# Kernel optimization log

Measured on AMD Instinct MI355X. Metric: run time of the kernel, lower is better.

The kernel has to match this reference:

```python
import jax, jax.numpy as jnp
import numpy as np

EPS = 1e-3
D_MODEL = 512
SEQ = 1024
BATCH = 4
N_LAYERS = 2
N_HEAD = 8
D_HEAD = 64
D_INNER = 1024


def _position_table(n_pos, d):
    # Faithful to PositionEncoding: sin applied to even cols; the cos line in
    # the source is a no-op (missing assignment), so odd cols stay raw.
    j = np.arange(d)
    pos = np.arange(n_pos)[:, None]
    pe = pos / np.power(10000.0, 2 * (j // 2) / d)
    pe[0] = 0.0
    pe[1:, 0::2] = np.sin(pe[1:, 0::2])
    return jnp.asarray(pe, dtype=jnp.float32)


def _layer_norm(z, a, b):
    # torch.std is unbiased (ddof=1); eps added to sigma, not variance
    mu = jnp.mean(z, axis=-1, keepdims=True)
    sigma = jnp.sqrt(jnp.sum((z - mu) ** 2, axis=-1, keepdims=True) / (z.shape[-1] - 1))
    return (z - mu) / (sigma + EPS) * a + b


def setup_inputs() -> dict:
    key = jax.random.key(0)
    ks = jax.random.split(key, 10)
    s = 0.02
    return {
        "x": jax.random.normal(ks[0], (BATCH, SEQ, D_MODEL), dtype=jnp.float32),
        "pos_enc": _position_table(SEQ, D_MODEL),
        "w_qs": jax.random.normal(ks[1], (N_LAYERS, N_HEAD, D_MODEL, D_HEAD), dtype=jnp.float32) * s,
        "w_ks": jax.random.normal(ks[2], (N_LAYERS, N_HEAD, D_MODEL, D_HEAD), dtype=jnp.float32) * s,
        "w_vs": jax.random.normal(ks[3], (N_LAYERS, N_HEAD, D_MODEL, D_HEAD), dtype=jnp.float32) * s,
        "ln1_a": jnp.ones((N_LAYERS, D_MODEL), dtype=jnp.float32),
        "ln1_b": jnp.zeros((N_LAYERS, D_MODEL), dtype=jnp.float32),
        "w1": jax.random.normal(ks[4], (N_LAYERS, D_INNER, D_MODEL), dtype=jnp.float32) * s,
        "b1": jax.random.normal(ks[5], (N_LAYERS, D_INNER), dtype=jnp.float32) * s,
        "w2": jax.random.normal(ks[6], (N_LAYERS, D_MODEL, D_INNER), dtype=jnp.float32) * s,
        "b2": jax.random.normal(ks[7], (N_LAYERS, D_MODEL), dtype=jnp.float32) * s,
        "ln2_a": jnp.ones((N_LAYERS, D_MODEL), dtype=jnp.float32),
        "ln2_b": jnp.zeros((N_LAYERS, D_MODEL), dtype=jnp.float32),
    }


def reference(x, pos_enc, w_qs, w_ks, w_vs, ln1_a, ln1_b, w1, b1, w2, b2, ln2_a, ln2_b):
    temper = jnp.sqrt(jnp.float32(D_MODEL))  # scale uses d_model, not d_k (as in source)
    x = x + pos_enc[None, :, :]
    for i in range(N_LAYERS):
        residual = x
        # per-head projections: [h, b, l, dk]
        q = jnp.einsum('bld,hdk->hblk', x, w_qs[i])
        k = jnp.einsum('bld,hdk->hblk', x, w_ks[i])
        v = jnp.einsum('bld,hdv->hblv', x, w_vs[i])
        attn = jax.nn.softmax(jnp.einsum('hbqk,hbmk->hbqm', q, k) / temper, axis=-1)
        out = jnp.einsum('hbqm,hbmv->hbqv', attn, v)
        # permute(1,2,0,3): concat heads along feature dim -> [b, l, h*dv]
        out = out.transpose(1, 2, 0, 3).reshape(BATCH, SEQ, N_HEAD * D_HEAD)
        x = _layer_norm(out + residual, ln1_a[i], ln1_b[i])
        # positionwise FFN (1x1 convs == linears)
        h = jax.nn.relu(jnp.einsum('bld,fd->blf', x, w1[i]) + b1[i])
        o = jnp.einsum('blf,df->bld', h, w2[i]) + b2[i]
        x = _layer_norm(o + x, ln2_a[i], ln2_b[i])
    return x
```

## Files before the change

### kernel.cpp

```cpp
#include <hip/hip_runtime.h>
#include <math.h>

#define D_MODEL 512
#define SEQ     1024
#define BATCH   4
#define N_LAYERS 2
#define N_HEAD  8
#define D_HEAD  64
#define D_INNER 1024
#define NTOK    (BATCH*SEQ)
#define LN_EPS  1e-3f

typedef float f32x4 __attribute__((ext_vector_type(4)));
typedef short bf16x8 __attribute__((ext_vector_type(8)));
typedef unsigned short ushort_t;
typedef unsigned int uint_t;
typedef unsigned long long ull_t;

__device__ inline ushort_t f2bf(float f) {
    uint_t u = __float_as_uint(f);
    u += 0x7FFFu + ((u >> 16) & 1u);
    return (ushort_t)(u >> 16);
}
__device__ inline float bf2f(ushort_t h) {
    return __uint_as_float((uint_t)h << 16);
}

__device__ __forceinline__ void gload16(const ushort_t* g, ushort_t* l) {
    __builtin_amdgcn_global_load_lds(
        (const __attribute__((address_space(1))) void*)g,
        (__attribute__((address_space(3))) void*)l, 16, 0, 0);
}

#define PREP_E0 (NTOK * D_MODEL)
#define PREP_E1 (1536 * 512)
#define PREP_EW (N_LAYERS * D_INNER * D_MODEL)
#define PREP_TOTAL (PREP_E0 + 2 * PREP_E1 + 2 * PREP_EW)

__global__ void prep_kernel(const float* __restrict__ x,
                            const float* __restrict__ pe,
                            const float* __restrict__ w_qs,
                            const float* __restrict__ w_ks,
                            const float* __restrict__ w_vs,
                            const float* __restrict__ w1,
                            const float* __restrict__ w2,
                            float* __restrict__ X,
                            ushort_t* __restrict__ Xraw,
                            ushort_t* __restrict__ Wqkv,
                            ushort_t* __restrict__ WqkvL,
                            ushort_t* __restrict__ W1b,
                            ushort_t* __restrict__ W2b) {
    int idx = blockIdx.x * 256 + threadIdx.x;
    if (idx < PREP_E0) {
        int l = (idx / D_MODEL) % SEQ;
        int d = idx % D_MODEL;
        float xv = x[idx];
        X[idx] = xv + pe[l * D_MODEL + d];
        Xraw[idx] = f2bf(xv);
        return;
    }
    idx -= PREP_E0;
    if (idx < 2 * PREP_E1) {
        int layer = idx / PREP_E1;
        int j = idx - layer * PREP_E1;
        int n = j >> 9, k = j & 511;
        int which = n >> 9, h = (n >> 6) & 7, d = n & 63;
        size_t wofs = (size_t)layer * N_HEAD * D_MODEL * D_HEAD;
        const float* W = (which == 0) ? w_qs + wofs
                       : (which == 1) ? w_ks + wofs : w_vs + wofs;
        float v = W[((size_t)h * D_MODEL + k) * D_HEAD + d];
        ushort_t hv = f2bf(v);
        Wqkv[(size_t)layer * PREP_E1 + j] = hv;
        if (layer == 0) WqkvL[j] = f2bf(v - bf2f(hv));
        return;
    }
    idx -= 2 * PREP_E1;
    if (idx < PREP_EW) { W1b[idx] = f2bf(w1[idx]); return; }
    idx -= PREP_EW;
    W2b[idx] = f2bf(w2[idx]);
}

__device__ inline void qkv_scatter(f32x4 a, int n, int m_base,
                                   const float* __restrict__ pew,
                                   ushort_t* Qhi, ushort_t* Qlo,
                                   ushort_t* Khi, ushort_t* Klo,
                                   ushort_t* Vt) {
    int which = n >> 9, hd = n & 511;
    int head = hd >> 6, d = hd & 63;
    int hb = head * BATCH + (m_base >> 10);
    int l  = m_base & 1023;
    if (pew) {
#pragma unroll
        for (int r = 0; r < 4; r++) a[r] += pew[(size_t)(l + r) * 1536 + n];
    }
    if (which == 2) {
        ushort4 pk = make_ushort4(f2bf(a[0]), f2bf(a[1]), f2bf(a[2]), f2bf(a[3]));
        *(ushort4*)(Vt + ((size_t)hb * D_HEAD + d) * SEQ + l) = pk;
    } else {
        ushort_t* H = (which == 0) ? Qhi : Khi;
        ushort_t* L = (which == 0) ? Qlo : Klo;
#pragma unroll
        for (int r = 0; r < 4; r++) {
            float v = a[r];
            ushort_t hv = f2bf(v);
            size_t off = ((size_t)hb * SEQ + l + r) * D_HEAD + d;
            H[off] = hv;
            L[off] = f2bf(v - bf2f(hv));
        }
    }
}

template<int MODE, int TM, int TN>
__global__ __launch_bounds__(256, (TM == 128 ? 3 : 4))
void gemm_kernel(const ushort_t* __restrict__ A, const ushort_t* __restrict__ Bt,
                 const float* __restrict__ bias, const float* __restrict__ pew,
                 float* __restrict__ outF, ushort_t* __restrict__ outB,
                 ushort_t* __restrict__ Qhi, ushort_t* __restrict__ Qlo,
                 ushort_t* __restrict__ Khi, ushort_t* __restrict__ Klo,
                 ushort_t* __restrict__ Vt,
                 int M, int N, int K) {
    constexpr int BK = 128;
    constexpr int WM = TM / 2, WN = TN / 2;
    constexpr int MT = WM / 16, NT = WN / 16;
    constexpr int WA = TM / 16;
    constexpr int WB = TN / 16;
    __shared__ ushort_t As[TM * BK];
    __shared__ ushort_t Bs[TN * BK];
    const int tid = threadIdx.x;
    const int m0 = blockIdx.y * TM, n0 = blockIdx.x * TN;
    const int w = tid >> 6, lane = tid & 63;
    const int wr = w >> 1, wc = w & 1;
    const int col = lane & 15, quad = lane >> 4;
    const int srow = lane >> 4;
    const int scc  = lane & 15;

    f32x4 acc[MT][NT] = {};

    for (int k0 = 0; k0 < K; k0 += BK) {
        __syncthreads();
#pragma unroll
        for (int q = 0; q < WA; q++) {
            int row = (w * WA + q) * 4 + srow;
            int sch = scc ^ (row & 7);
            gload16(A + (size_t)(m0 + row) * K + k0 + sch * 8,
                    &As[(w * WA + q) * 4 * BK]);
        }
#pragma unroll
        for (int q = 0; q < WB; q++) {
            int row = (w * WB + q) * 4 + srow;
            int sch = scc ^ (row & 7);
            gload16(Bt + (size_t)(n0 + row) * K + k0 + sch * 8,
                    &Bs[(w * WB + q) * 4 * BK]);
        }
        __syncthreads();
#pragma unroll
        for (int ks = 0; ks < BK; ks += 32) {
            const int cb = ks >> 3;
            const int sc_ = ((cb + quad) ^ (col & 7)) * 8;
            bf16x8 af[MT], bfr[NT];
#pragma unroll
            for (int t = 0; t < MT; t++)
                af[t] = *(const bf16x8*)(&As[(wr * WM + t * 16 + col) * BK + sc_]);
#pragma unroll
            for (int t = 0; t < NT; t++)
                bfr[t] = *(const bf16x8*)(&Bs[(wc * WN + t * 16 + col) * BK + sc_]);
#pragma unroll
            for (int mt = 0; mt < MT; mt++)
#pragma unroll
                for (int nt = 0; nt < NT; nt++)
                    acc[mt][nt] = __builtin_amdgcn_mfma_f32_16x16x32_bf16(
                        af[mt], bfr[nt], acc[mt][nt], 0, 0, 0);
        }
    }

#pragma unroll
    for (int mt = 0; mt < MT; mt++) {
#pragma unroll
        for (int nt = 0; nt < NT; nt++) {
            int n = n0 + wc * WN + nt * 16 + col;
            int m_base = m0 + wr * WM + mt * 16 + quad * 4;
            if (MODE == 0) {
                qkv_scatter(acc[mt][nt], n, m_base, pew, Qhi, Qlo, Khi, Klo, Vt);
            } else {
#pragma unroll
                for (int r = 0; r < 4; r++) {
                    int m = m_base + r;
                    float v = acc[mt][nt][r];
                    if (MODE == 1) {
                        float t = fmaxf(v + bias[n], 0.f);
                        outB[(size_t)m * N + n] = f2bf(t);
                    } else {
                        outF[(size_t)m * N + n] = v + bias[n];
                    }
                }
            }
        }
    }
}

__global__ __launch_bounds__(256, 4)
void gemm_hilo_kernel(const float* __restrict__ A,
                      const ushort_t* __restrict__ Bh,
                      const ushort_t* __restrict__ Bl,
                      float* __restrict__ outF, int M, int N, int K) {
    __shared__ ushort_t Ash[64][72];
    __shared__ ushort_t Asl[64][72];
    __shared__ ushort_t Bsh[64][72];
    __shared__ ushort_t Bsl[64][72];
    const int tid = threadIdx.x;
    const int m0 = blockIdx.y * 64, n0 = blockIdx.x * 64;
    const int w = tid >> 6, lane = tid & 63;
    const int wm = (w >> 1) * 32, wn = (w & 1) * 32;
    const int col = lane & 15, quad = lane >> 4;

    f32x4 acc[2][2] = {};

    for (int k0 = 0; k0 < K; k0 += 64) {
        __syncthreads();
#pragma unroll
        for (int p = 0; p < 4; p++) {
            int idx = p * 256 + tid;
            int row = idx >> 4, c4 = (idx & 15) * 4;
            float4 v = *(const float4*)(A + (size_t)(m0 + row) * K + k0 + c4);
            ushort_t h0 = f2bf(v.x), h1 = f2bf(v.y), h2 = f2bf(v.z), h3 = f2bf(v.w);
            *(ushort4*)(&Ash[row][c4]) = make_ushort4(h0, h1, h2, h3);
            *(ushort4*)(&Asl[row][c4]) = make_ushort4(
                f2bf(v.x - bf2f(h0)), f2bf(v.y - bf2f(h1)),
                f2bf(v.z - bf2f(h2)), f2bf(v.w - bf2f(h3)));
        }
#pragma unroll
        for (int p = 0; p < 2; p++) {
            int idx = p * 256 + tid;
            int row = idx >> 3, ch = (idx & 7) * 8;
            *(uint4*)(&Bsh[row][ch]) =
                *(const uint4*)(Bh + (size_t)(n0 + row) * K + k0 + ch);
            *(uint4*)(&Bsl[row][ch]) =
                *(const uint4*)(Bl + (size_t)(n0 + row) * K + k0 + ch);
        }
        __syncthreads();
#pragma unroll
        for (int ks = 0; ks < 64; ks += 32) {
            bf16x8 ah[2], al[2], bh[2], bl[2];
#pragma unroll
            for (int t = 0; t < 2; t++) {
                ah[t] = *(const bf16x8*)(&Ash[wm + t * 16 + col][ks + quad * 8]);
                al[t] = *(const bf16x8*)(&Asl[wm + t * 16 + col][ks + quad * 8]);
                bh[t] = *(const bf16x8*)(&Bsh[wn + t * 16 + col][ks + quad * 8]);
                bl[t] = *(const bf16x8*)(&Bsl[wn + t * 16 + col][ks + quad * 8]);
            }
#pragma unroll
            for (int mt = 0; mt < 2; mt++)
#pragma unroll
                for (int nt = 0; nt < 2; nt++) {
                    acc[mt][nt] = __builtin_amdgcn_mfma_f32_16x16x32_bf16(
                        ah[mt], bh[nt], acc[mt][nt], 0, 0, 0);
                    acc[mt][nt] = __builtin_amdgcn_mfma_f32_16x16x32_bf16(
                        ah[mt], bl[nt], acc[mt][nt], 0, 0, 0);
                    acc[mt][nt] = __builtin_amdgcn_mfma_f32_16x16x32_bf16(
                        al[mt], bh[nt], acc[mt][nt], 0, 0, 0);
                }
        }
    }

#pragma unroll
    for (int mt = 0; mt < 2; mt++)
#pragma unroll
        for (int nt = 0; nt < 2; nt++) {
            int n = n0 + wn + nt * 16 + col;
#pragma unroll
            for (int r = 0; r < 4; r++) {
                int m = m0 + wm + mt * 16 + quad * 4 + r;
                outF[(size_t)m * N + n] = acc[mt][nt][r];
            }
        }
}

template<bool HILO>
__global__ __launch_bounds__(256, 4)
void attention_kernel(const ushort_t* __restrict__ Qhi,
                      const ushort_t* __restrict__ Qlo,
                      const ushort_t* __restrict__ Khi,
                      const ushort_t* __restrict__ Klo,
                      const ushort_t* __restrict__ Vt,
                      float* __restrict__ P0,
                      float* __restrict__ P1,
                      float2* __restrict__ ML) {
    const int bid = blockIdx.x;
    const int split = bid >> 9;
    const int r9  = bid & 511;
    const int j   = r9 >> 3;
    const int hb  = (r9 & 7) * 4 + (j >> 4);
    const int qt  = j & 15;
    const int h = hb >> 2, b = hb & 3;
    const int tid = threadIdx.x;
    const int w = tid >> 6, lane = tid & 63;
    const int col = lane & 15, quad = lane >> 4;
    const size_t kbase = (size_t)hb * SEQ * D_HEAD;
    const size_t vbase = (size_t)hb * D_HEAD * SEQ;

    __shared__ ushort_t Kh[64][72];
    __shared__ ushort_t Kl[HILO ? 64 : 1][72];
    __shared__ ushort_t Vs[64][72];
    __shared__ ushort_t Pl[4][16][72];

    const int srow0 = tid >> 3;
    const int srow1 = 32 + (tid >> 3);
    const int sch   = (tid & 7) * 8;

    bf16x8 qh[2], ql[2];
    {
        const ushort_t* qp = Qhi + kbase + (size_t)(qt * 64 + w * 16 + col) * D_HEAD;
        qh[0] = *(const bf16x8*)(qp + quad * 8);
        qh[1] = *(const bf16x8*)(qp + 32 + quad * 8);
        if (HILO) {
            const ushort_t* lp = Qlo + kbase + (size_t)(qt * 64 + w * 16 + col) * D_HEAD;
            ql[0] = *(const bf16x8*)(lp + quad * 8);
            ql[1] = *(const bf16x8*)(lp + 32 + quad * 8);
        }
    }

    f32x4 acco[4] = {};
    float mrun = -1e30f, lrun = 0.f;
    const float inv_temper = 0.04419417382415922f;

    const int tbeg = split * (SEQ / 2);
    const int tend = tbeg + SEQ / 2;

    uint4 rK0, rK1, rL0, rL1, rV0, rV1;
    {
        const int t0 = tbeg;
        rK0 = *(const uint4*)(Khi + kbase + (size_t)(t0 + srow0) * D_HEAD + sch);
        rK1 = *(const uint4*)(Khi + kbase + (size_t)(t0 + srow1) * D_HEAD + sch);
        if (HILO) {
            rL0 = *(const uint4*)(Klo + kbase + (size_t)(t0 + srow0) * D_HEAD + sch);
            rL1 = *(const uint4*)(Klo + kbase + (size_t)(t0 + srow1) * D_HEAD + sch);
        }
        rV0 = *(const uint4*)(Vt + vbase + (size_t)srow0 * SEQ + t0 + sch);
        rV1 = *(const uint4*)(Vt + vbase + (size_t)srow1 * SEQ + t0 + sch);
    }

    for (int t0 = tbeg; t0 < tend; t0 += 64) {
        __syncthreads();
        *(uint4*)(&Kh[srow0][sch]) = rK0;
        *(uint4*)(&Kh[srow1][sch]) = rK1;
        if (HILO) {
            *(uint4*)(&Kl[srow0][sch]) = rL0;
            *(uint4*)(&Kl[srow1][sch]) = rL1;
        }
        *(uint4*)(&Vs[srow0][sch]) = rV0;
        *(uint4*)(&Vs[srow1][sch]) = rV1;
        __syncthreads();

        if (t0 + 64 < tend) {
            const int tn = t0 + 64;
            rK0 = *(const uint4*)(Khi + kbase + (size_t)(tn + srow0) * D_HEAD + sch);
            rK1 = *(const uint4*)(Khi + kbase + (size_t)(tn + srow1) * D_HEAD + sch);
            if (HILO) {
                rL0 = *(const uint4*)(Klo + kbase + (size_t)(tn + srow0) * D_HEAD + sch);
                rL1 = *(const uint4*)(Klo + kbase + (size_t)(tn + srow1) * D_HEAD + sch);
            }
            rV0 = *(const uint4*)(Vt + vbase + (size_t)srow0 * SEQ + tn + sch);
            rV1 = *(const uint4*)(Vt + vbase + (size_t)srow1 * SEQ + tn + sch);
        }

        float sc[4][4];
#pragma unroll
        for (int nt = 0; nt < 4; nt++) {
            bf16x8 kh0 = *(const bf16x8*)(&Kh[nt * 16 + col][quad * 8]);
            bf16x8 kh1 = *(const bf16x8*)(&Kh[nt * 16 + col][32 + quad * 8]);
            f32x4 s = {};
            s = __builtin_amdgcn_mfma_f32_16x16x32_bf16(kh0, qh[0], s, 0, 0, 0);
            s = __builtin_amdgcn_mfma_f32_16x16x32_bf16(kh1, qh[1], s, 0, 0, 0);
            if (HILO) {
                bf16x8 kl0 = *(const bf16x8*)(&Kl[nt * 16 + col][quad * 8]);
                bf16x8 kl1 = *(const bf16x8*)(&Kl[nt * 16 + col][32 + quad * 8]);
                s = __builtin_amdgcn_mfma_f32_16x16x32_bf16(kl0, qh[0], s, 0, 0, 0);
                s = __builtin_amdgcn_mfma_f32_16x16x32_bf16(kl1, qh[1], s, 0, 0, 0);
                s = __builtin_amdgcn_mfma_f32_16x16x32_bf16(kh0, ql[0], s, 0, 0, 0);
                s = __builtin_amdgcn_mfma_f32_16x16x32_bf16(kh1, ql[1], s, 0, 0, 0);
            }
#pragma unroll
            for (int r = 0; r < 4; r++) sc[nt][r] = s[r] * inv_temper;
        }

        bf16x8 va0[4], va1[4];
#pragma unroll
        for (int nt = 0; nt < 4; nt++) {
            va0[nt] = *(const bf16x8*)(&Vs[nt * 16 + col][quad * 8]);
            va1[nt] = *(const bf16x8*)(&Vs[nt * 16 + col][32 + quad * 8]);
        }

        float tmax = sc[0][0];
#pragma unroll
        for (int nt = 0; nt < 4; nt++)
#pragma unroll
            for (int r = 0; r < 4; r++) tmax = fmaxf(tmax, sc[nt][r]);
        tmax = fmaxf(tmax, __shfl_xor(tmax, 16, 64));
        tmax = fmaxf(tmax, __shfl_xor(tmax, 32, 64));

        float mn = fmaxf(mrun, tmax);
        float alpha = __expf(mrun - mn);
        mrun = mn;
        float tsum = 0.f;
#pragma unroll
        for (int nt = 0; nt < 4; nt++) {
            float p0 = __expf(sc[nt][0] - mn);
            float p1 = __expf(sc[nt][1] - mn);
            float p2 = __expf(sc[nt][2] - mn);
            float p3 = __expf(sc[nt][3] - mn);
            tsum += (p0 + p1) + (p2 + p3);
            ull_t pk = (ull_t)f2bf(p0) | ((ull_t)f2bf(p1) << 16)
                     | ((ull_t)f2bf(p2) << 32) | ((ull_t)f2bf(p3) << 48);
            *(ull_t*)(&Pl[w][col][nt * 16 + quad * 4]) = pk;
        }
        tsum += __shfl_xor(tsum, 16, 64);
        tsum += __shfl_xor(tsum, 32, 64);
        lrun = lrun * alpha + tsum;
#pragma unroll
        for (int nt = 0; nt < 4; nt++)
#pragma unroll
            for (int r = 0; r < 4; r++) acco[nt][r] *= alpha;

        __threadfence_block();

        union { ulong2 u; bf16x8 v; } pa0, pa1;
        pa0.u = *(const ulong2*)(&Pl[w][col][quad * 8]);
        pa1.u = *(const ulong2*)(&Pl[w][col][32 + quad * 8]);
#pragma unroll
        for (int nt = 0; nt < 4; nt++) {
            acco[nt] = __builtin_amdgcn_mfma_f32_16x16x32_bf16(va0[nt], pa0.v, acco[nt], 0, 0, 0);
            acco[nt] = __builtin_amdgcn_mfma_f32_16x16x32_bf16(va1[nt], pa1.v, acco[nt], 0, 0, 0);
        }
    }

    const int qrow = qt * 64 + w * 16 + col;
    float* dst = split ? P1 : P0;
#pragma unroll
    for (int nt = 0; nt < 4; nt++)
        *(f32x4*)(&dst[((size_t)b * SEQ + qrow) * D_MODEL + h * D_HEAD
                       + nt * 16 + quad * 4]) = acco[nt];
    if (quad == 0)
        ML[((size_t)split * 32 + hb) * SEQ + qrow] = make_float2(mrun, lrun);
}

__device__ inline float block_sum_256(float v, float* tmp) {
#pragma unroll
    for (int off = 32; off > 0; off >>= 1) v += __shfl_down(v, off, 64);
    if ((threadIdx.x & 63) == 0) tmp[threadIdx.x >> 6] = v;
    __syncthreads();
    return tmp[0] + tmp[1] + tmp[2] + tmp[3];
}

__global__ void add_norm_kernel(const float* __restrict__ A,
                                const float* __restrict__ R,
                                const float* __restrict__ ga,
                                const float* __restrict__ gb,
                                float* __restrict__ Out,
                                ushort_t* __restrict__ OutBf) {
    int tok = blockIdx.x, tid = threadIdx.x;
    __shared__ float t1[4], t2[4];
    size_t base = (size_t)tok * D_MODEL;
    float z0 = A[base + tid]       + R[base + tid];
    float z1 = A[base + tid + 256] + R[base + tid + 256];
    float s = block_sum_256(z0 + z1, t1);
    float mu = s * (1.f / (float)D_MODEL);
    float d0 = z0 - mu, d1 = z1 - mu;
    float ss = block_sum_256(d0 * d0 + d1 * d1, t2);
    float sigma = sqrtf(ss * (1.f / (float)(D_MODEL - 1)));
    float inv = 1.f / (sigma + LN_EPS);
    float r0 = d0 * inv * ga[tid]       + gb[tid];
    float r1 = d1 * inv * ga[tid + 256] + gb[tid + 256];
    Out[base + tid]         = r0;
    Out[base + tid + 256]   = r1;
    OutBf[base + tid]       = f2bf(r0);
    OutBf[base + tid + 256] = f2bf(r1);
}

__global__ void add_norm_combine_kernel(const float* __restrict__ Pa,
                                        const float* __restrict__ Pb,
                                        const float2* __restrict__ ML,
                                        const float* __restrict__ R,
                                        const float* __restrict__ ga,
                                        const float* __restrict__ gb,
                                        float* __restrict__ Out,
                                        ushort_t* __restrict__ OutBf) {
    int tok = blockIdx.x, tid = threadIdx.x;
    int b = tok >> 10, l = tok & 1023;
    __shared__ float t1[4], t2[4];
    int h0 = tid >> 6;
    float s0a, s0b, s1a, s1b;
    {
        int hb0 = h0 * 4 + b;
        float2 u0 = ML[(size_t)hb0 * SEQ + l];
        float2 u1 = ML[(size_t)(32 + hb0) * SEQ + l];
        float M = fmaxf(u0.x, u1.x);
        float e0 = __expf(u0.x - M), e1 = __expf(u1.x - M);
        float inv = 1.f / (e0 * u0.y + e1 * u1.y);
        s0a = e0 * inv; s0b = e1 * inv;
        int hb1 = (h0 + 4) * 4 + b;
        float2 v0 = ML[(size_t)hb1 * SEQ + l];
        float2 v1 = ML[(size_t)(32 + hb1) * SEQ + l];
        float M2 = fmaxf(v0.x, v1.x);
        float f0 = __expf(v0.x - M2), f1 = __expf(v1.x - M2);
        float inv2 = 1.f / (f0 * v0.y + f1 * v1.y);
        s1a = f0 * inv2; s1b = f1 * inv2;
    }
    size_t base = (size_t)tok * D_MODEL;
    float z0 = Pa[base + tid] * s0a + Pb[base + tid] * s0b + R[base + tid];
    float z1 = Pa[base + tid + 256] * s1a + Pb[base + tid + 256] * s1b
             + R[base + tid + 256];
    float s = block_sum_256(z0 + z1, t1);
    float mu = s * (1.f / (float)D_MODEL);
    float d0 = z0 - mu, d1 = z1 - mu;
    float ss = block_sum_256(d0 * d0 + d1 * d1, t2);
    float sigma = sqrtf(ss * (1.f / (float)(D_MODEL - 1)));
    float inv = 1.f / (sigma + LN_EPS);
    float r0 = d0 * inv * ga[tid]       + gb[tid];
    float r1 = d1 * inv * ga[tid + 256] + gb[tid + 256];
    Out[base + tid]         = r0;
    Out[base + tid + 256]   = r1;
    OutBf[base + tid]       = f2bf(r0);
    OutBf[base + tid + 256] = f2bf(r1);
}

extern "C" void kernel_launch(void* const* d_in, const int* in_sizes, int n_in,
                              void* d_out, int out_size, void* d_ws, size_t ws_size,
                              hipStream_t stream) {
    const float* x     = (const float*)d_in[0];
    const float* pe    = (const float*)d_in[1];
    const float* w_qs  = (const float*)d_in[2];
    const float* w_ks  = (const float*)d_in[3];
    const float* w_vs  = (const float*)d_in[4];
    const float* ln1_a = (const float*)d_in[5];
    const float* ln1_b = (const float*)d_in[6];
    const float* w1    = (const float*)d_in[7];
    const float* b1    = (const float*)d_in[8];
    const float* w2    = (const float*)d_in[9];
    const float* b2    = (const float*)d_in[10];
    const float* ln2_a = (const float*)d_in[11];
    const float* ln2_b = (const float*)d_in[12];
    float* out = (float*)d_out;

    const size_t NXD = (size_t)NTOK * D_MODEL;
    char* p = (char*)d_ws;
    float*    X    = (float*)p;     p += NXD * 4;
    float*    Ob   = (float*)p;     p += NXD * 4;
    ushort_t* Xbf  = (ushort_t*)p;  p += NXD * 2;
    ushort_t* Xraw = (ushort_t*)p;  p += NXD * 2;
    ushort_t* Qhi  = (ushort_t*)p;  p += NXD * 2;
    ushort_t* Qlo  = (ushort_t*)p;  p += NXD * 2;
    ushort_t* Khi  = (ushort_t*)p;  p += NXD * 2;
    ushort_t* Klo  = (ushort_t*)p;  p += NXD * 2;
    ushort_t* Vt   = (ushort_t*)p;  p += NXD * 2;
    ushort_t* Wqkv = (ushort_t*)p;  p += (size_t)N_LAYERS * 1536 * 512 * 2;
    ushort_t* WqkvL= (ushort_t*)p;  p += (size_t)1536 * 512 * 2;
    ushort_t* W1b  = (ushort_t*)p;  p += (size_t)N_LAYERS * D_INNER * D_MODEL * 2;
    ushort_t* W2b  = (ushort_t*)p;  p += (size_t)N_LAYERS * D_MODEL * D_INNER * 2;
    float2*   ML   = (float2*)p;
    ushort_t* Hbf  = Qhi;
    float*    PEW  = Ob;

    prep_kernel<<<(PREP_TOTAL + 255) / 256, 256, 0, stream>>>(
        x, pe, w_qs, w_ks, w_vs, w1, w2, X, Xraw, Wqkv, WqkvL, W1b, W2b);

    for (int i = 0; i < N_LAYERS; i++) {
        if (i == 0) {
            gemm_hilo_kernel<<<dim3(1536 / 64, SEQ / 64), 256, 0, stream>>>(
                pe, Wqkv, WqkvL, PEW, SEQ, 1536, D_MODEL);
            gemm_kernel<0, 128, 64><<<dim3(1536 / 64, NTOK / 128), 256, 0, stream>>>(
                Xraw, Wqkv, nullptr, PEW, nullptr, nullptr,
                Qhi, Qlo, Khi, Klo, Vt, NTOK, 1536, D_MODEL);
            attention_kernel<true><<<1024, 256, 0, stream>>>(
                Qhi, Qlo, Khi, Klo, Vt, Ob, out, ML);
        } else {
            gemm_kernel<0, 128, 64><<<dim3(1536 / 64, NTOK / 128), 256, 0, stream>>>(
                Xbf, Wqkv + (size_t)i * 1536 * 512, nullptr, nullptr, nullptr,
                nullptr, Qhi, Qlo, Khi, Klo, Vt, NTOK, 1536, D_MODEL);
            attention_kernel<false><<<1024, 256, 0, stream>>>(
                Qhi, Qlo, Khi, Klo, Vt, Ob, out, ML);
        }

        add_norm_combine_kernel<<<NTOK, 256, 0, stream>>>(
            Ob, out, ML, X, ln1_a + i * D_MODEL, ln1_b + i * D_MODEL, X, Xbf);

        gemm_kernel<1, 128, 64><<<dim3(D_INNER / 64, NTOK / 128), 256, 0, stream>>>(
            Xbf, W1b + (size_t)i * D_INNER * D_MODEL, b1 + (size_t)i * D_INNER,
            nullptr, nullptr, Hbf, nullptr, nullptr, nullptr, nullptr, nullptr,
            NTOK, D_INNER, D_MODEL);

        gemm_kernel<2, 64, 64><<<dim3(D_MODEL / 64, NTOK / 64), 256, 0, stream>>>(
            Hbf, W2b + (size_t)i * D_MODEL * D_INNER, b2 + (size_t)i * D_MODEL,
            nullptr, Ob, nullptr, nullptr, nullptr, nullptr, nullptr, nullptr,
            NTOK, D_MODEL, D_INNER);

        float* dst = (i == N_LAYERS - 1) ? out : X;
        add_norm_kernel<<<NTOK, 256, 0, stream>>>(
            Ob, X, ln2_a + i * D_MODEL, ln2_b + i * D_MODEL, dst, Xbf);
    }
}
```

Measured before the change: 272.7 us.

## Process two query sub-tiles per wave in attention to reuse K/V tiles

Each wave now handles 32 query rows (two 16-row sub-tiles) instead of 16, so a block covers 128 queries and the grid halves from 1024 to 512 blocks. Each K/V tile staged in shared memory and each K/V fragment read from LDS now feeds twice as many MFMAs, cutting global and LDS traffic per query. In exchange, register pressure rises (launch bounds drop to 2 blocks per CU) and there are fewer blocks to fill the GPU, which may reduce occupancy and latency hiding.

```diff
diff --git a/kernel.cpp b/kernel.cpp
--- a/kernel.cpp
+++ b/kernel.cpp
@@ -276,7 +276,7 @@
 }
 
 template<bool HILO>
-__global__ __launch_bounds__(256, 4)
+__global__ __launch_bounds__(256, 2)
 void attention_kernel(const ushort_t* __restrict__ Qhi,
                       const ushort_t* __restrict__ Qlo,
                       const ushort_t* __restrict__ Khi,
@@ -286,11 +286,11 @@
                       float* __restrict__ P1,
                       float2* __restrict__ ML) {
     const int bid = blockIdx.x;
-    const int split = bid >> 9;
-    const int r9  = bid & 511;
-    const int j   = r9 >> 3;
-    const int hb  = (r9 & 7) * 4 + (j >> 4);
-    const int qt  = j & 15;
+    const int split = bid >> 8;
+    const int r8  = bid & 255;
+    const int j   = r8 >> 3;
+    const int hb  = (r8 & 7) * 4 + (j >> 3);
+    const int qp2 = j & 7;
     const int h = hb >> 2, b = hb & 3;
     const int tid = threadIdx.x;
     const int w = tid >> 6, lane = tid & 63;
@@ -301,26 +301,28 @@
     __shared__ ushort_t Kh[64][72];
     __shared__ ushort_t Kl[HILO ? 64 : 1][72];
     __shared__ ushort_t Vs[64][72];
-    __shared__ ushort_t Pl[4][16][72];
+    __shared__ ushort_t Pl[4][2][16][72];
 
     const int srow0 = tid >> 3;
     const int srow1 = 32 + (tid >> 3);
     const int sch   = (tid & 7) * 8;
 
-    bf16x8 qh[2], ql[2];
-    {
-        const ushort_t* qp = Qhi + kbase + (size_t)(qt * 64 + w * 16 + col) * D_HEAD;
-        qh[0] = *(const bf16x8*)(qp + quad * 8);
-        qh[1] = *(const bf16x8*)(qp + 32 + quad * 8);
+    const int qbase = qp2 * 128 + w * 32;
+    bf16x8 qh[2][2], ql[2][2];
+#pragma unroll
+    for (int u = 0; u < 2; u++) {
+        const ushort_t* qp = Qhi + kbase + (size_t)(qbase + u * 16 + col) * D_HEAD;
+        qh[u][0] = *(const bf16x8*)(qp + quad * 8);
+        qh[u][1] = *(const bf16x8*)(qp + 32 + quad * 8);
         if (HILO) {
-            const ushort_t* lp = Qlo + kbase + (size_t)(qt * 64 + w * 16 + col) * D_HEAD;
-            ql[0] = *(const bf16x8*)(lp + quad * 8);
-            ql[1] = *(const bf16x8*)(lp + 32 + quad * 8);
-        }
-    }
-
-    f32x4 acco[4] = {};
-    float mrun = -1e30f, lrun = 0.f;
+            const ushort_t* lp = Qlo + kbase + (size_t)(qbase + u * 16 + col) * D_HEAD;
+            ql[u][0] = *(const bf16x8*)(lp + quad * 8);
+            ql[u][1] = *(const bf16x8*)(lp + 32 + quad * 8);
+        }
+    }
+
+    f32x4 acco[2][4] = {};
+    float mrun[2] = {-1e30f, -1e30f}, lrun[2] = {0.f, 0.f};
     const float inv_temper = 0.04419417382415922f;
 
     const int tbeg = split * (SEQ / 2);
@@ -363,84 +365,99 @@
             rV1 = *(const uint4*)(Vt + vbase + (size_t)srow1 * SEQ + tn + sch);
         }
 
-        float sc[4][4];
+        float sc[2][4][4];
 #pragma unroll
         for (int nt = 0; nt < 4; nt++) {
             bf16x8 kh0 = *(const bf16x8*)(&Kh[nt * 16 + col][quad * 8]);
             bf16x8 kh1 = *(const bf16x8*)(&Kh[nt * 16 + col][32 + quad * 8]);
-            f32x4 s = {};
-            s = __builtin_amdgcn_mfma_f32_16x16x32_bf16(kh0, qh[0], s, 0, 0, 0);
-            s = __builtin_amdgcn_mfma_f32_16x16x32_bf16(kh1, qh[1], s, 0, 0, 0);
+            f32x4 s0 = {}, s1 = {};
+            s0 = __builtin_amdgcn_mfma_f32_16x16x32_bf16(kh0, qh[0][0], s0, 0, 0, 0);
+            s0 = __builtin_amdgcn_mfma_f32_16x16x32_bf16(kh1, qh[0][1], s0, 0, 0, 0);
+            s1 = __builtin_amdgcn_mfma_f32_16x16x32_bf16(kh0, qh[1][0], s1, 0, 0, 0);
+            s1 = __builtin_amdgcn_mfma_f32_16x16x32_bf16(kh1, qh[1][1], s1, 0, 0, 0);
             if (HILO) {
                 bf16x8 kl0 = *(const bf16x8*)(&Kl[nt * 16 + col][quad * 8]);
                 bf16x8 kl1 = *(const bf16x8*)(&Kl[nt * 16 + col][32 + quad * 8]);
-                s = __builtin_amdgcn_mfma_f32_16x16x32_bf16(kl0, qh[0], s, 0, 0, 0);
-                s = __builtin_amdgcn_mfma_f32_16x16x32_bf16(kl1, qh[1], s, 0, 0, 0);
-                s = __builtin_amdgcn_mfma_f32_16x16x32_bf16(kh0, ql[0], s, 0, 0, 0);
-                s = __builtin_amdgcn_mfma_f32_16x16x32_bf16(kh1, ql[1], s, 0, 0, 0);
+                s0 = __builtin_amdgcn_mfma_f32_16x16x32_bf16(kl0, qh[0][0], s0, 0, 0, 0);
+                s0 = __builtin_amdgcn_mfma_f32_16x16x32_bf16(kl1, qh[0][1], s0, 0, 0, 0);
+                s0 = __builtin_amdgcn_mfma_f32_16x16x32_bf16(kh0, ql[0][0], s0, 0, 0, 0);
+                s0 = __builtin_amdgcn_mfma_f32_16x16x32_bf16(kh1, ql[0][1], s0, 0, 0, 0);
+                s1 = __builtin_amdgcn_mfma_f32_16x16x32_bf16(kl0, qh[1][0], s1, 0, 0, 0);
+                s1 = __builtin_amdgcn_mfma_f32_16x16x32_bf16(kl1, qh[1][1], s1, 0, 0, 0);
+                s1 = __builtin_amdgcn_mfma_f32_16x16x32_bf16(kh0, ql[1][0], s1, 0, 0, 0);
+                s1 = __builtin_amdgcn_mfma_f32_16x16x32_bf16(kh1, ql[1][1], s1, 0, 0, 0);
             }
 #pragma unroll
-            for (int r = 0; r < 4; r++) sc[nt][r] = s[r] * inv_temper;
-        }
-
-        bf16x8 va0[4], va1[4];
+            for (int r = 0; r < 4; r++) {
+                sc[0][nt][r] = s0[r] * inv_temper;
+                sc[1][nt][r] = s1[r] * inv_temper;
+            }
+        }
+
+#pragma unroll
+        for (int u = 0; u < 2; u++) {
+            float tmax = sc[u][0][0];
+#pragma unroll
+            for (int nt = 0; nt < 4; nt++)
+#pragma unroll
+                for (int r = 0; r < 4; r++) tmax = fmaxf(tmax, sc[u][nt][r]);
+            tmax = fmaxf(tmax, __shfl_xor(tmax, 16, 64));
+            tmax = fmaxf(tmax, __shfl_xor(tmax, 32, 64));
+
+            float mn = fmaxf(mrun[u], tmax);
+            float alpha = __expf(mrun[u] - mn);
+            mrun[u] = mn;
+            float tsum = 0.f;
+#pragma unroll
+            for (int nt = 0; nt < 4; nt++) {
+                float p0 = __expf(sc[u][nt][0] - mn);
+                float p1 = __expf(sc[u][nt][1] - mn);
+                float p2 = __expf(sc[u][nt][2] - mn);
+                float p3 = __expf(sc[u][nt][3] - mn);
+                tsum += (p0 + p1) + (p2 + p3);
+                ull_t pk = (ull_t)f2bf(p0) | ((ull_t)f2bf(p1) << 16)
+                         | ((ull_t)f2bf(p2) << 32) | ((ull_t)f2bf(p3) << 48);
+                *(ull_t*)(&Pl[w][u][col][nt * 16 + quad * 4]) = pk;
+            }
+            tsum += __shfl_xor(tsum, 16, 64);
+            tsum += __shfl_xor(tsum, 32, 64);
+            lrun[u] = lrun[u] * alpha + tsum;
+#pragma unroll
+            for (int nt = 0; nt < 4; nt++)
+#pragma unroll
+                for (int r = 0; r < 4; r++) acco[u][nt][r] *= alpha;
+        }
+
+        __threadfence_block();
+
+        union { ulong2 uu; bf16x8 v; } pa[2][2];
+#pragma unroll
+        for (int u = 0; u < 2; u++) {
+            pa[u][0].uu = *(const ulong2*)(&Pl[w][u][col][quad * 8]);
+            pa[u][1].uu = *(const ulong2*)(&Pl[w][u][col][32 + quad * 8]);
+        }
 #pragma unroll
         for (int nt = 0; nt < 4; nt++) {
-            va0[nt] = *(const bf16x8*)(&Vs[nt * 16 + col][quad * 8]);
-            va1[nt] = *(const bf16x8*)(&Vs[nt * 16 + col][32 + quad * 8]);
-        }
-
-        float tmax = sc[0][0];
+            bf16x8 bv0 = *(const bf16x8*)(&Vs[nt * 16 + col][quad * 8]);
+            bf16x8 bv1 = *(const bf16x8*)(&Vs[nt * 16 + col][32 + quad * 8]);
+            acco[0][nt] = __builtin_amdgcn_mfma_f32_16x16x32_bf16(bv0, pa[0][0].v, acco[0][nt], 0, 0, 0);
+            acco[0][nt] = __builtin_amdgcn_mfma_f32_16x16x32_bf16(bv1, pa[0][1].v, acco[0][nt], 0, 0, 0);
+            acco[1][nt] = __builtin_amdgcn_mfma_f32_16x16x32_bf16(bv0, pa[1][0].v, acco[1][nt], 0, 0, 0);
+            acco[1][nt] = __builtin_amdgcn_mfma_f32_16x16x32_bf16(bv1, pa[1][1].v, acco[1][nt], 0, 0, 0);
+        }
+    }
+
+    float* dst = split ? P1 : P0;
+#pragma unroll
+    for (int u = 0; u < 2; u++) {
+        const int qrow = qbase + u * 16 + col;
 #pragma unroll
         for (int nt = 0; nt < 4; nt++)
-#pragma unroll
-            for (int r = 0; r < 4; r++) tmax = fmaxf(tmax, sc[nt][r]);
-        tmax = fmaxf(tmax, __shfl_xor(tmax, 16, 64));
-        tmax = fmaxf(tmax, __shfl_xor(tmax, 32, 64));
-
-        float mn = fmaxf(mrun, tmax);
-        float alpha = __expf(mrun - mn);
-        mrun = mn;
-        float tsum = 0.f;
-#pragma unroll
-        for (int nt = 0; nt < 4; nt++) {
-            float p0 = __expf(sc[nt][0] - mn);
-            float p1 = __expf(sc[nt][1] - mn);
-            float p2 = __expf(sc[nt][2] - mn);
-            float p3 = __expf(sc[nt][3] - mn);
-            tsum += (p0 + p1) + (p2 + p3);
-            ull_t pk = (ull_t)f2bf(p0) | ((ull_t)f2bf(p1) << 16)
-                     | ((ull_t)f2bf(p2) << 32) | ((ull_t)f2bf(p3) << 48);
-            *(ull_t*)(&Pl[w][col][nt * 16 + quad * 4]) = pk;
-        }
-        tsum += __shfl_xor(tsum, 16, 64);
-        tsum += __shfl_xor(tsum, 32, 64);
-        lrun = lrun * alpha + tsum;
-#pragma unroll
-        for (int nt = 0; nt < 4; nt++)
-#pragma unroll
-            for (int r = 0; r < 4; r++) acco[nt][r] *= alpha;
-
-        __threadfence_block();
-
-        union { ulong2 u; bf16x8 v; } pa0, pa1;
-        pa0.u = *(const ulong2*)(&Pl[w][col][quad * 8]);
-        pa1.u = *(const ulong2*)(&Pl[w][col][32 + quad * 8]);
-#pragma unroll
-        for (int nt = 0; nt < 4; nt++) {
-            acco[nt] = __builtin_amdgcn_mfma_f32_16x16x32_bf16(va0[nt], pa0.v, acco[nt], 0, 0, 0);
-            acco[nt] = __builtin_amdgcn_mfma_f32_16x16x32_bf16(va1[nt], pa1.v, acco[nt], 0, 0, 0);
-        }
-    }
-
-    const int qrow = qt * 64 + w * 16 + col;
-    float* dst = split ? P1 : P0;
-#pragma unroll
-    for (int nt = 0; nt < 4; nt++)
-        *(f32x4*)(&dst[((size_t)b * SEQ + qrow) * D_MODEL + h * D_HEAD
-                       + nt * 16 + quad * 4]) = acco[nt];
-    if (quad == 0)
-        ML[((size_t)split * 32 + hb) * SEQ + qrow] = make_float2(mrun, lrun);
+            *(f32x4*)(&dst[((size_t)b * SEQ + qrow) * D_MODEL + h * D_HEAD
+                           + nt * 16 + quad * 4]) = acco[u][nt];
+        if (quad == 0)
+            ML[((size_t)split * 32 + hb) * SEQ + qrow] = make_float2(mrun[u], lrun[u]);
+    }
 }
 
 __device__ inline float block_sum_256(float v, float* tmp) {
@@ -570,13 +587,13 @@
             gemm_kernel<0, 128, 64><<<dim3(1536 / 64, NTOK / 128), 256, 0, stream>>>(
                 Xraw, Wqkv, nullptr, PEW, nullptr, nullptr,
                 Qhi, Qlo, Khi, Klo, Vt, NTOK, 1536, D_MODEL);
-            attention_kernel<true><<<1024, 256, 0, stream>>>(
+            attention_kernel<true><<<512, 256, 0, stream>>>(
                 Qhi, Qlo, Khi, Klo, Vt, Ob, out, ML);
         } else {
             gemm_kernel<0, 128, 64><<<dim3(1536 / 64, NTOK / 128), 256, 0, stream>>>(
                 Xbf, Wqkv + (size_t)i * 1536 * 512, nullptr, nullptr, nullptr,
                 nullptr, Qhi, Qlo, Khi, Klo, Vt, NTOK, 1536, D_MODEL);
-            attention_kernel<false><<<1024, 256, 0, stream>>>(
+            attention_kernel<false><<<512, 256, 0, stream>>>(
                 Qhi, Qlo, Khi, Klo, Vt, Ob, out, ML);
         }
 
```

Measured after the change: 271.9 us. Within noise of the previous version (-0.3%).
